# Kernel tuning notes

Measured on AMD Instinct MI355X. Metric: run time of the kernel, lower is better.

Reference implementation:

```python
import jax, jax.numpy as jnp
import numpy as np

B, T, K = 64, 2000, 256
BLANK_LOGPROB = -1.0
NEG = jnp.float32(-1e30)  # stand-in for -inf, safe under logaddexp


def setup_inputs() -> dict:
    key = jax.random.key(0)
    k1, k2, k3 = jax.random.split(key, 3)
    attn_logprob = jax.random.normal(k1, (B, 1, T, K), dtype=jnp.float32)
    key_lens = jax.random.randint(k2, (B,), K // 2, K + 1)
    query_lens = jax.random.randint(k3, (B,), T // 2, T + 1)
    return {"attn_logprob": attn_logprob, "key_lens": key_lens, "query_lens": query_lens}


def _forward_sum(attn_logprob, key_lens, query_lens):
    # attn_logprob: [B, 1, T, K]; targets are 1..K_b (strictly increasing, all distinct)
    Bn, _, Tn, Kn = attn_logprob.shape
    logp = attn_logprob[:, 0]                                   # [B, T, K]
    # pad blank class at key index 0 (torch F.pad(pad=(1,0), value=blank_logprob))
    padded = jnp.pad(logp, ((0, 0), (0, 0), (1, 0)), constant_values=BLANK_LOGPROB)  # [B,T,K+1]
    # masked log_softmax over classes 0..K_b (matches per-sample slice [:key_lens+1])
    key_idx = jnp.arange(Kn + 1)
    key_mask = key_idx[None, :] <= key_lens[:, None]            # [B, K+1]
    masked = jnp.where(key_mask[:, None, :], padded, NEG)
    log_probs = jax.nn.log_softmax(masked, axis=-1)             # [B, T, K+1]

    # CTC forward DP. States s = 0..2K: even -> blank (class 0), odd -> label (s+1)//2.
    S = 2 * Kn + 1
    s_idx = jnp.arange(S)
    lab = jnp.where(s_idx % 2 == 0, 0, (s_idx + 1) // 2)        # class index per state
    # skip transition s-2 -> s allowed for odd s >= 3 (all labels distinct)
    skip_ok = (s_idx % 2 == 1) & (s_idx >= 3)

    emit0 = log_probs[:, 0, :][:, lab]                          # [B, S]
    alpha0 = jnp.full((Bn, S), NEG, dtype=log_probs.dtype)
    alpha0 = alpha0.at[:, 0].set(emit0[:, 0]).at[:, 1].set(emit0[:, 1])

    xs = jnp.moveaxis(log_probs[:, 1:, :], 1, 0)                # [T-1, B, K+1]
    ts = jnp.arange(1, Tn)

    def step(alpha, inp):
        x, t = inp
        emit = x[:, lab]                                        # [B, S]
        sh1 = jnp.concatenate([jnp.full((Bn, 1), NEG, alpha.dtype), alpha[:, :-1]], axis=1)
        sh2 = jnp.concatenate([jnp.full((Bn, 2), NEG, alpha.dtype), alpha[:, :-2]], axis=1)
        sh2 = jnp.where(skip_ok[None, :], sh2, NEG)
        new = jnp.logaddexp(jnp.logaddexp(alpha, sh1), sh2) + emit
        # freeze alpha once t >= query_lens[b] so final carry = alpha at t = T_b - 1
        return jnp.where((t < query_lens)[:, None], new, alpha), None

    alpha_final, _ = jax.lax.scan(step, alpha0, (xs, ts))       # [B, S]

    last = 2 * key_lens                                          # final state index per sample
    a_last = jnp.take_along_axis(alpha_final, last[:, None], axis=1)[:, 0]
    a_prev = jnp.take_along_axis(alpha_final, (last - 1)[:, None], axis=1)[:, 0]
    nll = -jnp.logaddexp(a_last, a_prev)                         # per-sample CTC NLL
    # torch CTCLoss(reduction='mean') on a batch of 1: divide by target length
    loss = nll / jnp.maximum(key_lens, 1).astype(nll.dtype)
    loss = jnp.where(nll > 0.5e30, 0.0, loss)                    # zero_infinity
    return jnp.mean(loss)


def reference(attn_logprob, key_lens, query_lens):
    return _forward_sum(attn_logprob, key_lens, query_lens)
```

## Files before the change

### kernel.cpp

```cpp
#include <hip/hip_runtime.h>
#include <cstdint>
#include <cstddef>

#define BB    64
#define TB    2000
#define KB    256

constexpr float LOG2E = 1.4426950408889634f;
constexpr float LN2f  = 0.6931471805599453f;
constexpr float WBF   = 0.36787944117144233f;

__device__ __forceinline__ float exp2i(int k) {
  return __uint_as_float((uint32_t)(127 + k) << 23);
}
__device__ __forceinline__ float shr1z(float v) {
  return __int_as_float(__builtin_amdgcn_update_dpp(
      0, __float_as_int(v), 0x138, 0xF, 0xF, true));
}
__device__ __forceinline__ float dmax64(float v) {
#define DSTEP(ctrl, rm, bc)                                                  \
  { float t = __int_as_float(__builtin_amdgcn_update_dpp(                    \
        __float_as_int(v), __float_as_int(v), (ctrl), (rm), 0xF, (bc)));     \
    v = fmaxf(v, t); }
  DSTEP(0x111, 0xF, true) DSTEP(0x112, 0xF, true) DSTEP(0x114, 0xF, true)
  DSTEP(0x118, 0xF, true) DSTEP(0x142, 0xA, false) DSTEP(0x143, 0xC, false)
#undef DSTEP
  return __int_as_float(__builtin_amdgcn_readlane(__float_as_int(v), 63));
}
__device__ __forceinline__ float dsum64(float v) {
#define DSTEP(ctrl, rm, bc)                                                  \
  { float t = __int_as_float(__builtin_amdgcn_update_dpp(                    \
        __float_as_int(v), __float_as_int(v), (ctrl), (rm), 0xF, (bc)));     \
    v += t; }
  DSTEP(0x111, 0xF, true) DSTEP(0x112, 0xF, true) DSTEP(0x114, 0xF, true)
  DSTEP(0x118, 0xF, true) DSTEP(0x142, 0xA, false) DSTEP(0x143, 0xC, false)
#undef DSTEP
  return v;
}
__device__ __forceinline__ float wsum64(float v) {
#pragma unroll
  for (int m = 32; m >= 1; m >>= 1) v += __shfl_xor(v, m, 64);
  return v;
}

__global__ __launch_bounds__(256)
void fsl_main(const float* __restrict__ x, const int* __restrict__ key_lens,
              const int* __restrict__ query_lens, float* __restrict__ partial,
              float* __restrict__ alast, float* __restrict__ aprev) {
  __shared__ __align__(16) char ring[65536];
  __shared__ int prodG[3];
  __shared__ int consG;

  const int tid  = threadIdx.x;
  const int b    = blockIdx.x;
  const int lane = tid & 63;
  const int w    = tid >> 6;
  const int kl   = key_lens[b];
  const int qlen = query_lens[b];
  const int total = qlen - 1;
  const int ng    = (total + 7) >> 3;
  const float* xb  = x + (size_t)b * (TB * KB);
  const char*  xbc = (const char*)xb;
  const int lane16 = lane << 4;

  if (tid == 0) { prodG[0] = 0; prodG[1] = 0; prodG[2] = 0; consG = 0; }
  __syncthreads();

  if (w == 0) {
    float a0 = 0.f, a1 = 0.f, a2 = 0.f, a3 = 0.f;
    float b0 = 0.f, b1 = 0.f, b2 = 0.f, b3 = 0.f, s512 = 0.f;
    if (lane == 0) { a0 = WBF; b0 = __builtin_amdgcn_exp2f(xb[0] * LOG2E); }
    int Cw = 0;
    float m_red = dmax64(fmaxf(a0, b0));

    float4 e0, e1, e2, e3, e4, e5, e6, e7;
    float4 f0, f1, f2, f3, f4, f5, f6, f7;
    volatile int* vp0 = &prodG[0];
    volatile int* vp1 = &prodG[1];
    volatile int* vp2 = &prodG[2];

#define POLL(GN) do {                                                        \
    const int tgt_ = (GN);                                                   \
    int c0_ = *vp0, c1_ = *vp1, c2_ = *vp2;                                  \
    while (min(c0_, min(c1_, c2_)) < tgt_) {                                 \
      __builtin_amdgcn_s_sleep(2);                                           \
      c0_ = *vp0; c1_ = *vp1; c2_ = *vp2;                                    \
    }                                                                        \
    __asm__ __volatile__("" ::: "memory");                                   \
  } while (0)

#define LD8(E, g) do {                                                       \
    const char* sb_ = ring + (((g) & 7) << 13) + lane16;                     \
    E##0 = *(const float4*)(sb_);                                            \
    E##1 = *(const float4*)(sb_ + 1024);                                     \
    E##2 = *(const float4*)(sb_ + 2048);                                     \
    E##3 = *(const float4*)(sb_ + 3072);                                     \
    E##4 = *(const float4*)(sb_ + 4096);                                     \
    E##5 = *(const float4*)(sb_ + 5120);                                     \
    E##6 = *(const float4*)(sb_ + 6144);                                     \
    E##7 = *(const float4*)(sb_ + 7168);                                     \
  } while (0)

#define STEP1(EV) do {                                                       \
    const float pm1 = shr1z(b3);                                             \
    const float t0_ = a0 + pm1;                                              \
    const float t1_ = a1 + b0;                                               \
    const float t2_ = a2 + b1;                                               \
    const float t3_ = a3 + b2;                                               \
    s512 = s512 + b3;                                                        \
    b0 = (b0 + t0_) * EV.x;                                                  \
    b1 = (b1 + t1_) * EV.y;                                                  \
    b2 = (b2 + t2_) * EV.z;                                                  \
    b3 = (b3 + t3_) * EV.w;                                                  \
    a0 = t0_; a1 = t1_; a2 = t2_; a3 = t3_;                                  \
  } while (0)

#define STEP1G(EV, J) do { if ((J) < rem) { STEP1(EV); } } while (0)

#define RUN8(E)  do { STEP1(E##0); STEP1(E##1); STEP1(E##2); STEP1(E##3);    \
                      STEP1(E##4); STEP1(E##5); STEP1(E##6); STEP1(E##7); } while (0)
#define RUN8G(E) do { STEP1G(E##0,0); STEP1G(E##1,1); STEP1G(E##2,2);        \
                      STEP1G(E##3,3); STEP1G(E##4,4); STEP1G(E##5,5);        \
                      STEP1G(E##6,6); STEP1G(E##7,7); } while (0)

#define APPLY() do {                                                         \
    int e_ = (int)((__float_as_uint(m_red) >> 23) & 0xFF) - 127;             \
    if (!(m_red > 0.f)) e_ = -24;                                            \
    const int k_ = e_ + 24;                      \
    if (k_ > 126) {                                                          \
      const int kh_ = k_ >> 1;                                               \
      const float s1_ = exp2i(-kh_), s2_ = exp2i(-(k_ - kh_));               \
      a0 *= s1_; a1 *= s1_; a2 *= s1_; a3 *= s1_;                            \
      b0 *= s1_; b1 *= s1_; b2 *= s1_; b3 *= s1_; s512 *= s1_;               \
      a0 *= s2_; a1 *= s2_; a2 *= s2_; a3 *= s2_;                            \
      b0 *= s2_; b1 *= s2_; b2 *= s2_; b3 *= s2_; s512 *= s2_;               \
    } else {                                                                 \
      const float s_ = exp2i(-k_);                                           \
      a0 *= s_; a1 *= s_; a2 *= s_; a3 *= s_;                                \
      b0 *= s_; b1 *= s_; b2 *= s_; b3 *= s_; s512 *= s_;                    \
    }                                                                        \
    Cw += k_;                                                                \
  } while (0)

#define MEASURE() do {                                                       \
    float ml_ = fmaxf(fmaxf(fmaxf(a0, a1), fmaxf(a2, a3)),                   \
                      fmaxf(fmaxf(b0, b1), fmaxf(b2, b3)));                  \
    ml_ = fmaxf(ml_, s512);                                                  \
    m_red = dmax64(ml_);                                                     \
  } while (0)

    POLL(2);
    LD8(e, 0); LD8(f, 1);
    int cg = 0;
    for (;;) {
      if (8 * cg + 8 <= total) { RUN8(e); }
      else { const int rem = total - 8 * cg; RUN8G(e); }
      APPLY(); MEASURE();
      if (cg + 2 < ng) { POLL(cg + 3); LD8(e, cg + 2); }
      if (cg + 1 < ng) {
        if (8 * cg + 16 <= total) { RUN8(f); }
        else { const int rem = total - 8 * cg - 8; RUN8G(f); }
        APPLY(); MEASURE();
      }
      if (cg + 3 < ng) { POLL(cg + 4); LD8(f, cg + 3); }
      __asm__ __volatile__("" ::: "memory");
      if (lane == 0) *(volatile int*)&consG = cg + 4;
      cg += 2;
      if (cg >= ng) break;
    }
#undef POLL
#undef LD8
#undef STEP1
#undef STEP1G
#undef RUN8
#undef RUN8G
#undef APPLY
#undef MEASURE

    float* ev = (float*)ring;
    float* od = (float*)(ring + 4096);
    *(float4*)(ev + (lane << 2)) = make_float4(a0, a1, a2, a3);
    *(float4*)(od + (lane << 2)) = make_float4(b0, b1, b2, b3);
    if (lane == 63) *(float*)(ring + 8192) = s512;
    __asm__ __volatile__("" ::: "memory");
    if (lane == 0) {
      const float aL = (kl < 256) ? ev[kl] : *(float*)(ring + 8192);
      const float aP = od[kl - 1];
      const float dC = (float)Cw - (float)total * LOG2E;
      alast[b] = (log2f(aL) + dC) * LN2f;
      aprev[b] = (log2f(aP) + dC) * LN2f;
    }
  } else {
    const int pw = w - 1;
    const int c0 = lane << 2;
    const float bs0 = (c0 + 0 < kl) ? LOG2E : -20000.f;
    const float bs1 = (c0 + 1 < kl) ? LOG2E : -20000.f;
    const float bs2 = (c0 + 2 < kl) ? LOG2E : -20000.f;
    const float bs3 = (c0 + 3 < kl) ? LOG2E : -20000.f;
    volatile int* vc = &consG;
    float acc = 0.f;

    if (pw == 0) {
      const float4 v = *(const float4*)(xbc + lane16);
      float s_ = __builtin_amdgcn_exp2f(fmaf(v.x, LOG2E, bs0))
               + __builtin_amdgcn_exp2f(fmaf(v.y, LOG2E, bs1))
               + __builtin_amdgcn_exp2f(fmaf(v.z, LOG2E, bs2))
               + __builtin_amdgcn_exp2f(fmaf(v.w, LOG2E, bs3));
      s_ = dsum64(s_);
      acc += __builtin_amdgcn_logf((s_ + 1.0f) * WBF);
    }

    float4 A0, A1, A2, A3, A4, A5, A6, A7;
    float4 B0, B1, B2, B3, B4, B5, B6, B7;
    float4 C0, C1, C2, C3, C4, C5, C6, C7;

#define LOADG(P, GG) do {                                                    \
    const int rb_ = 8 * (GG) + 1;                                            \
    P##0 = *(const float4*)(xbc + (size_t)min(rb_ + 0, TB - 1) * 1024 + lane16); \
    P##1 = *(const float4*)(xbc + (size_t)min(rb_ + 1, TB - 1) * 1024 + lane16); \
    P##2 = *(const float4*)(xbc + (size_t)min(rb_ + 2, TB - 1) * 1024 + lane16); \
    P##3 = *(const float4*)(xbc + (size_t)min(rb_ + 3, TB - 1) * 1024 + lane16); \
    P##4 = *(const float4*)(xbc + (size_t)min(rb_ + 4, TB - 1) * 1024 + lane16); \
    P##5 = *(const float4*)(xbc + (size_t)min(rb_ + 5, TB - 1) * 1024 + lane16); \
    P##6 = *(const float4*)(xbc + (size_t)min(rb_ + 6, TB - 1) * 1024 + lane16); \
    P##7 = *(const float4*)(xbc + (size_t)min(rb_ + 7, TB - 1) * 1024 + lane16); \
  } while (0)

#define PR1(V, J) do {                                                       \
    float4 wv_;                                                              \
    wv_.x = __builtin_amdgcn_exp2f(fmaf(V.x, LOG2E, bs0));                   \
    wv_.y = __builtin_amdgcn_exp2f(fmaf(V.y, LOG2E, bs1));                   \
    wv_.z = __builtin_amdgcn_exp2f(fmaf(V.z, LOG2E, bs2));                   \
    wv_.w = __builtin_amdgcn_exp2f(fmaf(V.w, LOG2E, bs3));                   \
    *(float4*)(dstb_ + ((J) << 10)) = wv_;                                   \
    if (rb_ + (J) <= total) {                                                \
      float sr_ = (wv_.x + wv_.y) + (wv_.z + wv_.w);                         \
      sr_ = dsum64(sr_);                                                     \
      acc += __builtin_amdgcn_logf((sr_ + 1.0f) * WBF);                      \
    }                                                                        \
  } while (0)

#define PROC(P, GG) do {                                                     \
    const int rb_ = 8 * (GG) + 1;                                            \
    if ((GG) >= 8) {                                    \
      int c_ = *vc;                                                          \
      while (c_ < (GG) - 7) { __builtin_amdgcn_s_sleep(2); c_ = *vc; }       \
      __asm__ __volatile__("" ::: "memory");                                 \
    }                                                                        \
    char* dstb_ = ring + (((GG) & 7) << 13) + lane16;                        \
    PR1(P##0, 0); PR1(P##1, 1); PR1(P##2, 2); PR1(P##3, 3);                  \
    PR1(P##4, 4); PR1(P##5, 5); PR1(P##6, 6); PR1(P##7, 7);                  \
    __asm__ __volatile__("s_waitcnt lgkmcnt(0)" ::: "memory");               \
    if (lane == 0) *(volatile int*)&prodG[pw] = (GG) + 3;                    \
  } while (0)

    LOADG(A, pw); LOADG(B, pw + 3);
    int g = pw;
    for (;;) {
      LOADG(C, g + 6);
      PROC(A, g);
      g += 3; if (g >= ng) break;
      LOADG(A, g + 6);
      PROC(B, g);
      g += 3; if (g >= ng) break;
      LOADG(B, g + 6);
      PROC(C, g);
      g += 3; if (g >= ng) break;
    }
#undef LOADG
#undef PR1
#undef PROC
    __asm__ __volatile__("" ::: "memory");
    if (lane == 0) *(volatile int*)&prodG[pw] = 0x7fffffff;
    if (lane == 63) partial[4 * b + pw] = acc;
  }
}

__global__ __launch_bounds__(64)
void fsl_finish(const float* __restrict__ partial, const int* __restrict__ key_lens,
                const float* __restrict__ alast, const float* __restrict__ aprev,
                float* __restrict__ out) {
  const int b = threadIdx.x;
  const float SumLse =
      ((partial[4 * b] + partial[4 * b + 1]) + partial[4 * b + 2]) * LN2f;
  const float al = alast[b], ap = aprev[b];
  const float mx = fmaxf(al, ap);
  const float lae = (mx == -INFINITY) ? -INFINITY
                                      : mx + log1pf(expf(-fabsf(al - ap)));
  const float nll = SumLse - lae;
  const int kl = key_lens[b];
  float lv = nll / (float)max(kl, 1);
  if (nll > 5e29f) lv = 0.f;
  float v = wsum64(lv);
  if (b == 0) out[0] = v * (1.0f / 64.0f);
}

extern "C" void kernel_launch(void* const* d_in, const int* in_sizes, int n_in,
                              void* d_out, int out_size, void* d_ws, size_t ws_size,
                              hipStream_t stream) {
  const float* x     = (const float*)d_in[0];
  const int*   klens = (const int*)d_in[1];
  const int*   qlens = (const int*)d_in[2];
  float* out = (float*)d_out;

  float* partial = (float*)d_ws;
  float* alast   = partial + BB * 4;
  float* aprev   = alast + BB;

  fsl_main  <<<BB, 256, 0, stream>>>(x, klens, qlens, partial, alast, aprev);
  fsl_finish<<<1, 64, 0, stream>>>(partial, klens, alast, aprev, out);
}
```

Measured before the change: 143.2 us.

## Triple-buffer consumer register prefetch and poll producer flags with one vector load

The consumer wave now keeps three groups of eight timesteps in registers instead of two. It polls producer progress once per three groups with a single 16-byte LDS read of all flags, where before it read three separate volatile flags inside a sleep loop with a longer sleep. This is meant to hide LDS load latency and cut polling overhead on the serial DP critical path. The trade-off is more register pressure (24 float4 values) and a changed consumer release protocol (consG = cg+6), which must still stay consistent with the 8-slot ring and the producer logic.

```diff
diff --git a/kernel.cpp b/kernel.cpp
--- a/kernel.cpp
+++ b/kernel.cpp
@@ -48,7 +48,7 @@
               const int* __restrict__ query_lens, float* __restrict__ partial,
               float* __restrict__ alast, float* __restrict__ aprev) {
   __shared__ __align__(16) char ring[65536];
-  __shared__ int prodG[3];
+  __shared__ __align__(16) int prodG[4];
   __shared__ int consG;
 
   const int tid  = threadIdx.x;
@@ -63,7 +63,7 @@
   const char*  xbc = (const char*)xb;
   const int lane16 = lane << 4;
 
-  if (tid == 0) { prodG[0] = 0; prodG[1] = 0; prodG[2] = 0; consG = 0; }
+  if (tid == 0) { prodG[0] = 0; prodG[1] = 0; prodG[2] = 0; prodG[3] = 0x7fffffff; consG = 0; }
   __syncthreads();
 
   if (w == 0) {
@@ -75,16 +75,15 @@
 
     float4 e0, e1, e2, e3, e4, e5, e6, e7;
     float4 f0, f1, f2, f3, f4, f5, f6, f7;
-    volatile int* vp0 = &prodG[0];
-    volatile int* vp1 = &prodG[1];
-    volatile int* vp2 = &prodG[2];
+    float4 g0, g1, g2, g3, g4, g5, g6, g7;
 
 #define POLL(GN) do {                                                        \
     const int tgt_ = (GN);                                                   \
-    int c0_ = *vp0, c1_ = *vp1, c2_ = *vp2;                                  \
-    while (min(c0_, min(c1_, c2_)) < tgt_) {                                 \
-      __builtin_amdgcn_s_sleep(2);                                           \
-      c0_ = *vp0; c1_ = *vp1; c2_ = *vp2;                                    \
+    for (;;) {                                                               \
+      __asm__ __volatile__("" ::: "memory");                                 \
+      const int4 fl_ = *(const int4*)prodG;                                  \
+      if (min(fl_.x, min(fl_.y, fl_.z)) >= tgt_) break;                      \
+      __builtin_amdgcn_s_sleep(1);                                           \
     }                                                                        \
     __asm__ __volatile__("" ::: "memory");                                   \
   } while (0)
@@ -115,11 +114,12 @@
     a0 = t0_; a1 = t1_; a2 = t2_; a3 = t3_;                                  \
   } while (0)
 
-#define STEP1G(EV, J) do { if ((J) < rem) { STEP1(EV); } } while (0)
+#define STEP1G(EV, J) do { if ((J) < rem_) { STEP1(EV); } } while (0)
 
 #define RUN8(E)  do { STEP1(E##0); STEP1(E##1); STEP1(E##2); STEP1(E##3);    \
                       STEP1(E##4); STEP1(E##5); STEP1(E##6); STEP1(E##7); } while (0)
-#define RUN8G(E) do { STEP1G(E##0,0); STEP1G(E##1,1); STEP1G(E##2,2);        \
+#define RUN8G(E, RM) do { const int rem_ = (RM);                             \
+                      STEP1G(E##0,0); STEP1G(E##1,1); STEP1G(E##2,2);        \
                       STEP1G(E##3,3); STEP1G(E##4,4); STEP1G(E##5,5);        \
                       STEP1G(E##6,6); STEP1G(E##7,7); } while (0)
 
@@ -149,23 +149,32 @@
     m_red = dmax64(ml_);                                                     \
   } while (0)
 
-    POLL(2);
-    LD8(e, 0); LD8(f, 1);
+#define RUNGRP(E, G) do {                                                    \
+    if (8 * (G) + 8 <= total) { RUN8(E); }                                   \
+    else { RUN8G(E, total - 8 * (G)); }                                      \
+    APPLY(); MEASURE();                                                      \
+  } while (0)
+
+    POLL(3);
+    LD8(e, 0);
+    if (1 < ng) LD8(f, 1);
+    if (2 < ng) LD8(g, 2);
     int cg = 0;
     for (;;) {
-      if (8 * cg + 8 <= total) { RUN8(e); }
-      else { const int rem = total - 8 * cg; RUN8G(e); }
-      APPLY(); MEASURE();
-      if (cg + 2 < ng) { POLL(cg + 3); LD8(e, cg + 2); }
+      POLL(min(cg + 6, ng));
+      RUNGRP(e, cg);
+      if (cg + 3 < ng) LD8(e, cg + 3);
       if (cg + 1 < ng) {
-        if (8 * cg + 16 <= total) { RUN8(f); }
-        else { const int rem = total - 8 * cg - 8; RUN8G(f); }
-        APPLY(); MEASURE();
+        RUNGRP(f, cg + 1);
+        if (cg + 4 < ng) LD8(f, cg + 4);
       }
-      if (cg + 3 < ng) { POLL(cg + 4); LD8(f, cg + 3); }
+      if (cg + 2 < ng) {
+        RUNGRP(g, cg + 2);
+        if (cg + 5 < ng) LD8(g, cg + 5);
+      }
       __asm__ __volatile__("" ::: "memory");
-      if (lane == 0) *(volatile int*)&consG = cg + 4;
-      cg += 2;
+      if (lane == 0) *(volatile int*)&consG = cg + 6;
+      cg += 3;
       if (cg >= ng) break;
     }
 #undef POLL
@@ -176,6 +185,7 @@
 #undef RUN8G
 #undef APPLY
 #undef MEASURE
+#undef RUNGRP
 
     float* ev = (float*)ring;
     float* od = (float*)(ring + 4096);
```

After: 124.0 us. 13.4% less time.
